# Kernel tuning notes

Hardware: AMD Instinct MI355X
Metric: run time of the kernel (lower is better)

## Reference

```python
import jax, jax.numpy as jnp
import numpy as np

B = 32          # batch_size
S = 64          # num_subgraph
D = 8           # dim_multi_hot (module-level global in source repo)
NE = S * D      # num_edges = 512
NNODES = 1024
E = 150000      # incidence rows
IN_UNITS = [16, 32, 32]
OUT_UNITS = [32, 32, 16]


def _glorot(key, shape):
    # glorot_normal over last two dims (out, in)
    fan_out, fan_in = shape[-2], shape[-1]
    std = (2.0 / (fan_in + fan_out)) ** 0.5
    return std * jax.random.normal(key, shape, dtype=jnp.float32)


def setup_inputs() -> dict:
    key = jax.random.key(0)
    ks = jax.random.split(key, 10)
    nodes_features = jax.random.normal(ks[0], (NNODES * S, IN_UNITS[0]), dtype=jnp.float32)
    c0 = jax.random.randint(ks[1], (E,), 0, B, dtype=jnp.int32)
    c1 = jax.random.randint(ks[2], (E,), 0, NNODES, dtype=jnp.int32)
    c2 = jax.random.randint(ks[3], (E,), 0, S, dtype=jnp.int32)
    c3 = jax.random.randint(ks[4], (E,), 0, D, dtype=jnp.int32)
    incidence_matrix = jnp.stack([c0, c1, c2, c3], axis=1)
    return {
        'nodes_features': nodes_features,
        'in_core0': _glorot(ks[5], (NE, IN_UNITS[1], IN_UNITS[0])),
        'in_bias0': jnp.zeros((NE, IN_UNITS[1], 1), jnp.float32),
        'in_core1': _glorot(ks[6], (NE, IN_UNITS[2], IN_UNITS[1])),
        'in_bias1': jnp.zeros((NE, IN_UNITS[2], 1), jnp.float32),
        'out_core0': _glorot(ks[7], (NE, OUT_UNITS[1], OUT_UNITS[0])),
        'out_bias0': jnp.zeros((NE, OUT_UNITS[1], 1), jnp.float32),
        'out_core1': _glorot(ks[8], (NE, OUT_UNITS[2], OUT_UNITS[1])),
        'out_bias1': jnp.zeros((NE, OUT_UNITS[2], 1), jnp.float32),
        'incidence_matrix': incidence_matrix,
    }


def reference(nodes_features, in_core0, in_bias0, in_core1, in_bias1,
              out_core0, out_bias0, out_core1, out_bias1, incidence_matrix):
    c0 = incidence_matrix[:, 0]
    c1 = incidence_matrix[:, 1]
    c2 = incidence_matrix[:, 2]
    c3 = incidence_matrix[:, 3]

    # gather node features per incidence row: [E, in0]
    x = nodes_features[c1 * S + c2]
    eidx = c2 * D + c3  # per-edge weight index, < NE

    # per-edge MLP (gathered batched matmul + bias + relu)
    for W, b in ((in_core0, in_bias0), (in_core1, in_bias1)):
        x = jax.nn.relu(jnp.einsum('eoi,ei->eo', W[eidx], x) + b[eidx, :, 0])

    # unsorted segment mean over irregular edge groups
    seg = c0 * (D * S) + c2 * D + c3
    nseg = B * S * D
    sums = jax.ops.segment_sum(x, seg, num_segments=nseg)           # [B*NE, 32]
    cnt = jax.ops.segment_sum(jnp.ones((x.shape[0], 1), x.dtype), seg, num_segments=nseg)
    ef = jnp.where(cnt > 0, sums / jnp.maximum(cnt, 1.0), 0.0)       # [B*NE, 32]

    # output MLP: weights tiled over batch (einsum avoids explicit repeat)
    ef = ef.reshape(B, NE, -1)
    for W, b in ((out_core0, out_bias0), (out_core1, out_bias1)):
        ef = jax.nn.relu(jnp.einsum('eoi,bei->beo', W, ef) + b[None, :, :, 0])

    return ef.reshape(B * NE, OUT_UNITS[-1], 1)
```

## Files before the change

### kernel.cpp

```cpp
#include <hip/hip_runtime.h>

#define B_    32
#define S_    64
#define D_    8
#define NE_   512
#define E_    150000
#define CAP   448

#define SBLK  1024
#define BLKN  ((E_ + SBLK - 1) / SBLK)
#define SLOTS 16
#define PBIN_PITCH (BLKN * SLOTS)

#define PAYLOAD_BYTE_OFF (NE_ * BLKN * 4)

typedef __attribute__((ext_vector_type(8)))  short  short8;
typedef __attribute__((ext_vector_type(16))) float  float16;

__device__ __forceinline__ unsigned short f2bf(float f) {
    union { float f; unsigned int u; } cv; cv.f = f;
    unsigned int u = cv.u;
    return (unsigned short)((u + 0x7fffu + ((u >> 16) & 1u)) >> 16);
}
__device__ __forceinline__ unsigned int pack2bf(float a, float b) {
    return (unsigned int)f2bf(a) | ((unsigned int)f2bf(b) << 16);
}

__global__ __launch_bounds__(SBLK)
void scatter_bin(const int* __restrict__ inc,
                 int* __restrict__ cnt2D,
                 int* __restrict__ payload2D) {
    __shared__ int lcount[NE_];
    const int tid = threadIdx.x;

    for (int i = tid; i < NE_; i += SBLK) lcount[i] = 0;
    __syncthreads();

    const int e = blockIdx.x * SBLK + tid;
    int ei = -1, lp = 0, pl = 0;
    if (e < E_) {
        const int4 c = ((const int4*)inc)[e];
        ei = c.z * D_ + c.w;
        pl = (c.x << 16) | (c.y * S_ + c.z);
        lp = atomicAdd(&lcount[ei], 1);
    }
    if (ei >= 0 && lp < SLOTS)
        payload2D[ei * PBIN_PITCH + blockIdx.x * SLOTS + lp] = pl;
    __syncthreads();
    if (tid < NE_)
        cnt2D[tid * BLKN + blockIdx.x] = min(lcount[tid], SLOTS);
}

#define HLP 40

__global__ __launch_bounds__(512, 4)
void main_mfma(const float* __restrict__ nf,
               const float* __restrict__ iw0, const float* __restrict__ ib0,
               const float* __restrict__ iw1, const float* __restrict__ ib1,
               const float* __restrict__ ow0, const float* __restrict__ ob0,
               const float* __restrict__ ow1, const float* __restrict__ ob1,
               const int* __restrict__ cnt2D, const int* __restrict__ payload2D,
               float* __restrict__ out) {
    const int bid  = blockIdx.x;
    const int tid  = threadIdx.x;
    const int lane = tid & 63;
    const int wav  = tid >> 6;
    const int e32  = lane & 31;
    const int q    = lane >> 5;

    __shared__ float acc[32][33];
    __shared__ float hb[32][33];
    __shared__ float cnts[32];
    __shared__ float q0t[32 * 33];
    __shared__ float q1t[32 * 17];
    __shared__ float qb0s[32], qb1s[16];
    __shared__ float bias0s[32], bias1s[32];
    __shared__ int   scnt[256];
    __shared__ int   elist[CAP];
    __shared__ unsigned short Hl[8][32 * HLP];

    short8 aWa, aWb0, aWb1;
    {
        const float* wa = iw0 + (size_t)bid * 512 + e32 * 16 + q * 8;
        float4 u0 = ((const float4*)wa)[0], u1 = ((const float4*)wa)[1];
        unsigned int p[4] = { pack2bf(u0.x,u0.y), pack2bf(u0.z,u0.w),
                              pack2bf(u1.x,u1.y), pack2bf(u1.z,u1.w) };
        aWa = *(short8*)p;
    }
    {
        const float* wb = iw1 + (size_t)bid * 1024 + e32 * 32 + q * 8;
        float4 u0 = ((const float4*)wb)[0], u1 = ((const float4*)wb)[1];
        unsigned int p[4] = { pack2bf(u0.x,u0.y), pack2bf(u0.z,u0.w),
                              pack2bf(u1.x,u1.y), pack2bf(u1.z,u1.w) };
        aWb0 = *(short8*)p;
        const float* wb2 = wb + 16;
        float4 u2 = ((const float4*)wb2)[0], u3 = ((const float4*)wb2)[1];
        unsigned int p2[4] = { pack2bf(u2.x,u2.y), pack2bf(u2.z,u2.w),
                               pack2bf(u3.x,u3.y), pack2bf(u3.z,u3.w) };
        aWb1 = *(short8*)p2;
    }

    int mycnt = 0;
    if (tid < BLKN) mycnt = cnt2D[bid * BLKN + tid];
    if (tid < 256)  scnt[tid] = (tid < BLKN) ? mycnt : 0;

    for (int i = tid; i < 1024; i += 512) {
        const int o = i >> 5, k = i & 31;
        q0t[k * 33 + o] = ow0[(size_t)bid * 1024 + i];
    }
    { const int o = tid >> 5, k = tid & 31;
      q1t[k * 17 + o] = ow1[(size_t)bid * 512 + tid]; }
    if (tid < 32)       { bias0s[tid] = ib0[bid * 32 + tid]; cnts[tid] = 0.f; }
    else if (tid < 64)  bias1s[tid - 32] = ib1[bid * 32 + (tid - 32)];
    else if (tid < 96)  qb0s[tid - 64] = ob0[bid * 32 + (tid - 64)];
    else if (tid < 112) qb1s[tid - 96] = ob1[bid * 16 + (tid - 96)];
    for (int i = tid; i < 32 * 33; i += 512) ((float*)acc)[i] = 0.f;
    __syncthreads();

    #pragma unroll
    for (int off = 1; off < 256; off <<= 1) {
        int v = 0;
        if (tid < 256) { v = scnt[tid]; if (tid >= off) v += scnt[tid - off]; }
        __syncthreads();
        if (tid < 256) scnt[tid] = v;
        __syncthreads();
    }
    const int n = min(scnt[BLKN - 1], CAP);

    const int* Pb = payload2D + (size_t)bid * PBIN_PITCH;
    for (int pair = tid; pair < PBIN_PITCH; pair += 512) {
        const int blk = pair >> 4, s = pair & (SLOTS - 1);
        const int b0 = blk ? scnt[blk - 1] : 0;
        const int cc = scnt[blk] - b0;
        if (s < cc) {
            const int idx = b0 + s;
            if (idx < CAP) elist[idx] = Pb[pair];
        }
    }
    __syncthreads();

    const int ntiles = (n + 31) >> 5;
    unsigned short* hl = Hl[wav];

    for (int t = wav; t < ntiles; t += 8) {
        const int slot  = t * 32 + e32;
        const bool valid = slot < n;
        const int cs    = valid ? slot : (n - 1);

        const int p   = elist[cs];
        const int b_e = p >> 16;
        const int row = p & 0xFFFF;

        short8 bX;
        {
            const float4* xp = (const float4*)(nf + (size_t)row * 16 + q * 8);
            float4 u0 = xp[0], u1 = xp[1];
            unsigned int pk[4] = { pack2bf(u0.x,u0.y), pack2bf(u0.z,u0.w),
                                   pack2bf(u1.x,u1.y), pack2bf(u1.z,u1.w) };
            bX = *(short8*)pk;
        }

        float16 c0;
        #pragma unroll
        for (int r = 0; r < 16; ++r) {
            const int o_r = (r & 3) + 8 * (r >> 2) + 4 * q;
            c0[r] = bias0s[o_r];
        }
        c0 = __builtin_amdgcn_mfma_f32_32x32x16_bf16(aWa, bX, c0, 0, 0, 0);

        #pragma unroll
        for (int r = 0; r < 16; r += 2) {
            const int o_r = (r & 3) + 8 * (r >> 2) + 4 * q;
            const unsigned int pk = pack2bf(fmaxf(c0[r], 0.f), fmaxf(c0[r + 1], 0.f));
            *(unsigned int*)(hl + e32 * HLP + o_r) = pk;
        }

        short8 bH0 = *(const short8*)(hl + e32 * HLP + q * 8);
        short8 bH1 = *(const short8*)(hl + e32 * HLP + 16 + q * 8);
        float16 c1;
        #pragma unroll
        for (int r = 0; r < 16; ++r) {
            const int o_r = (r & 3) + 8 * (r >> 2) + 4 * q;
            c1[r] = bias1s[o_r];
        }
        c1 = __builtin_amdgcn_mfma_f32_32x32x16_bf16(aWb0, bH0, c1, 0, 0, 0);
        c1 = __builtin_amdgcn_mfma_f32_32x32x16_bf16(aWb1, bH1, c1, 0, 0, 0);

        if (valid) {
            #pragma unroll
            for (int r = 0; r < 16; ++r) {
                const int o_r = (r & 3) + 8 * (r >> 2) + 4 * q;
                atomicAdd(&acc[b_e][o_r], fmaxf(c1[r], 0.f));
            }
            if (q == 0) atomicAdd(&cnts[b_e], 1.f);
        }
    }
    __syncthreads();

    {
        const int b  = tid >> 4;
        const int j  = tid & 15;
        const float cv  = cnts[b];
        const float inv = cv > 0.f ? 1.0f / cv : 0.0f;
        #pragma unroll
        for (int s = 0; s < 2; ++s) {
            const int oo = j * 2 + s;
            float d = 0.f;
            #pragma unroll
            for (int k = 0; k < 32; ++k) d = fmaf(q0t[k * 33 + oo], acc[b][k], d);
            hb[b][oo] = fmaxf(fmaf(d, inv, qb0s[oo]), 0.f);
        }
    }
    __syncthreads();

    {
        const int b = tid >> 4;
        const int o = tid & 15;
        float d = qb1s[o];
        #pragma unroll
        for (int k = 0; k < 32; ++k) d = fmaf(q1t[k * 17 + o], hb[b][k], d);
        out[((size_t)b * NE_ + bid) * 16 + o] = fmaxf(d, 0.f);
    }
}

extern "C" void kernel_launch(void* const* d_in, const int* in_sizes, int n_in,
                              void* d_out, int out_size, void* d_ws, size_t ws_size,
                              hipStream_t stream) {
    const float* nf  = (const float*)d_in[0];
    const float* iw0 = (const float*)d_in[1];
    const float* ib0 = (const float*)d_in[2];
    const float* iw1 = (const float*)d_in[3];
    const float* ib1 = (const float*)d_in[4];
    const float* ow0 = (const float*)d_in[5];
    const float* ob0 = (const float*)d_in[6];
    const float* ow1 = (const float*)d_in[7];
    const float* ob1 = (const float*)d_in[8];
    const int*   inc = (const int*)d_in[9];

    int* cnt2D     = (int*)d_ws;
    int* payload2D = (int*)((char*)d_ws + PAYLOAD_BYTE_OFF);

    scatter_bin<<<BLKN, SBLK, 0, stream>>>(inc, cnt2D, payload2D);
    main_mfma<<<NE_, 512, 0, stream>>>(nf, iw0, ib0, iw1, ib1, ow0, ob0, ow1, ob1,
                                       cnt2D, payload2D, (float*)d_out);
}
```

Baseline: 118.4 us.

## Replace per-block bins with global-atomic CSR scatter and register-only MLP tiles

The scatter kernel now reserves contiguous slots per edge with one global atomicAdd per block and edge bin, writing a compact CAP-sized list per edge. This removes the prefix scan and compaction in the main kernel. The main kernel prefetches at most two tiles per wave up front. It replaces the LDS round-trip between the two MLP layers with v_permlane32_swap register shuffles. The changes add a memset launch and global atomics, and they assume at most 16 tiles per edge (n ≤ 448), which CAP enforces.

```diff
diff --git a/kernel.cpp b/kernel.cpp
--- a/kernel.cpp
+++ b/kernel.cpp
@@ -7,12 +7,8 @@
 #define E_    150000
 #define CAP   448
 
-#define SBLK  1024
-#define BLKN  ((E_ + SBLK - 1) / SBLK)
-#define SLOTS 16
-#define PBIN_PITCH (BLKN * SLOTS)
-
-#define PAYLOAD_BYTE_OFF (NE_ * BLKN * 4)
+#define SC_BLK  1024
+#define SC_GRID ((E_ + SC_BLK - 1) / SC_BLK)
 
 typedef __attribute__((ext_vector_type(8)))  short  short8;
 typedef __attribute__((ext_vector_type(16))) float  float16;
@@ -26,17 +22,18 @@
     return (unsigned int)f2bf(a) | ((unsigned int)f2bf(b) << 16);
 }
 
-__global__ __launch_bounds__(SBLK)
-void scatter_bin(const int* __restrict__ inc,
-                 int* __restrict__ cnt2D,
-                 int* __restrict__ payload2D) {
+__global__ __launch_bounds__(SC_BLK)
+void scatter_csr(const int* __restrict__ inc,
+                 int* __restrict__ gcnt,
+                 int* __restrict__ payload) {
     __shared__ int lcount[NE_];
+    __shared__ int lbase[NE_];
     const int tid = threadIdx.x;
 
-    for (int i = tid; i < NE_; i += SBLK) lcount[i] = 0;
-    __syncthreads();
-
-    const int e = blockIdx.x * SBLK + tid;
+    if (tid < NE_) lcount[tid] = 0;
+    __syncthreads();
+
+    const int e = blockIdx.x * SC_BLK + tid;
     int ei = -1, lp = 0, pl = 0;
     if (e < E_) {
         const int4 c = ((const int4*)inc)[e];
@@ -44,14 +41,54 @@
         pl = (c.x << 16) | (c.y * S_ + c.z);
         lp = atomicAdd(&lcount[ei], 1);
     }
-    if (ei >= 0 && lp < SLOTS)
-        payload2D[ei * PBIN_PITCH + blockIdx.x * SLOTS + lp] = pl;
-    __syncthreads();
-    if (tid < NE_)
-        cnt2D[tid * BLKN + blockIdx.x] = min(lcount[tid], SLOTS);
-}
-
-#define HLP 40
+    __syncthreads();
+
+    if (tid < NE_) {
+        const int c = lcount[tid];
+        lbase[tid] = c ? atomicAdd(&gcnt[tid], c) : 0;
+    }
+    __syncthreads();
+
+    if (ei >= 0) {
+        const int s = lbase[ei] + lp;
+        if (s < CAP) payload[ei * CAP + s] = pl;
+    }
+}
+
+
+#define TILE_COMPUTE(bXv, pvv, vldv)                                            \
+  {                                                                             \
+    float16 c0;                                                                 \
+    _Pragma("unroll")                                                           \
+    for (int r = 0; r < 16; ++r)                                                \
+        c0[r] = bias0s[(r & 3) + 8 * (r >> 2) + 4 * q];                         \
+    c0 = __builtin_amdgcn_mfma_f32_32x32x16_bf16(aWa, (bXv), c0, 0, 0, 0);      \
+    unsigned Pw[8];                                                             \
+    _Pragma("unroll")                                                           \
+    for (int j = 0; j < 8; ++j)                                                 \
+        Pw[j] = pack2bf(fmaxf(c0[2 * j], 0.f), fmaxf(c0[2 * j + 1], 0.f));      \
+    asm("v_permlane32_swap_b32 %0, %1" : "+v"(Pw[0]), "+v"(Pw[2]));             \
+    asm("v_permlane32_swap_b32 %0, %1" : "+v"(Pw[1]), "+v"(Pw[3]));             \
+    asm("v_permlane32_swap_b32 %0, %1" : "+v"(Pw[4]), "+v"(Pw[6]));             \
+    asm("v_permlane32_swap_b32 %0, %1" : "+v"(Pw[5]), "+v"(Pw[7]));             \
+    union { unsigned u[4]; short8 s; } H0c, H1c;                                \
+    H0c.u[0] = Pw[0]; H0c.u[1] = Pw[1]; H0c.u[2] = Pw[2]; H0c.u[3] = Pw[3];     \
+    H1c.u[0] = Pw[4]; H1c.u[1] = Pw[5]; H1c.u[2] = Pw[6]; H1c.u[3] = Pw[7];     \
+    float16 c1;                                                                 \
+    _Pragma("unroll")                                                           \
+    for (int r = 0; r < 16; ++r)                                                \
+        c1[r] = bias1s[(r & 3) + 8 * (r >> 2) + 4 * q];                         \
+    c1 = __builtin_amdgcn_mfma_f32_32x32x16_bf16(aWb0, H0c.s, c1, 0, 0, 0);     \
+    c1 = __builtin_amdgcn_mfma_f32_32x32x16_bf16(aWb1, H1c.s, c1, 0, 0, 0);     \
+    if (vldv) {                                                                 \
+        const int b_e = ((pvv) >> 16) & 31;                                     \
+        _Pragma("unroll")                                                       \
+        for (int r = 0; r < 16; ++r)                                            \
+            atomicAdd(&acc[b_e][(r & 3) + 8 * (r >> 2) + 4 * q],                \
+                      fmaxf(c1[r], 0.f));                                       \
+        if (q == 0) atomicAdd(&cnts[b_e], 1.f);                                 \
+    }                                                                           \
+  }
 
 __global__ __launch_bounds__(512, 4)
 void main_mfma(const float* __restrict__ nf,
@@ -59,7 +96,7 @@
                const float* __restrict__ iw1, const float* __restrict__ ib1,
                const float* __restrict__ ow0, const float* __restrict__ ob0,
                const float* __restrict__ ow1, const float* __restrict__ ob1,
-               const int* __restrict__ cnt2D, const int* __restrict__ payload2D,
+               const int* __restrict__ gcnt, const int* __restrict__ payload,
                float* __restrict__ out) {
     const int bid  = blockIdx.x;
     const int tid  = threadIdx.x;
@@ -75,9 +112,6 @@
     __shared__ float q1t[32 * 17];
     __shared__ float qb0s[32], qb1s[16];
     __shared__ float bias0s[32], bias1s[32];
-    __shared__ int   scnt[256];
-    __shared__ int   elist[CAP];
-    __shared__ unsigned short Hl[8][32 * HLP];
 
     short8 aWa, aWb0, aWb1;
     {
@@ -100,10 +134,6 @@
         aWb1 = *(short8*)p2;
     }
 
-    int mycnt = 0;
-    if (tid < BLKN) mycnt = cnt2D[bid * BLKN + tid];
-    if (tid < 256)  scnt[tid] = (tid < BLKN) ? mycnt : 0;
-
     for (int i = tid; i < 1024; i += 512) {
         const int o = i >> 5, k = i & 31;
         q0t[k * 33 + o] = ow0[(size_t)bid * 1024 + i];
@@ -115,86 +145,42 @@
     else if (tid < 96)  qb0s[tid - 64] = ob0[bid * 32 + (tid - 64)];
     else if (tid < 112) qb1s[tid - 96] = ob1[bid * 16 + (tid - 96)];
     for (int i = tid; i < 32 * 33; i += 512) ((float*)acc)[i] = 0.f;
-    __syncthreads();
-
-    #pragma unroll
-    for (int off = 1; off < 256; off <<= 1) {
-        int v = 0;
-        if (tid < 256) { v = scnt[tid]; if (tid >= off) v += scnt[tid - off]; }
-        __syncthreads();
-        if (tid < 256) scnt[tid] = v;
-        __syncthreads();
-    }
-    const int n = min(scnt[BLKN - 1], CAP);
-
-    const int* Pb = payload2D + (size_t)bid * PBIN_PITCH;
-    for (int pair = tid; pair < PBIN_PITCH; pair += 512) {
-        const int blk = pair >> 4, s = pair & (SLOTS - 1);
-        const int b0 = blk ? scnt[blk - 1] : 0;
-        const int cc = scnt[blk] - b0;
-        if (s < cc) {
-            const int idx = b0 + s;
-            if (idx < CAP) elist[idx] = Pb[pair];
-        }
-    }
-    __syncthreads();
-
+
+    const int n = min(gcnt[bid], CAP);
     const int ntiles = (n + 31) >> 5;
-    unsigned short* hl = Hl[wav];
-
-    for (int t = wav; t < ntiles; t += 8) {
-        const int slot  = t * 32 + e32;
-        const bool valid = slot < n;
-        const int cs    = valid ? slot : (n - 1);
-
-        const int p   = elist[cs];
-        const int b_e = p >> 16;
-        const int row = p & 0xFFFF;
-
-        short8 bX;
-        {
-            const float4* xp = (const float4*)(nf + (size_t)row * 16 + q * 8);
-            float4 u0 = xp[0], u1 = xp[1];
-            unsigned int pk[4] = { pack2bf(u0.x,u0.y), pack2bf(u0.z,u0.w),
-                                   pack2bf(u1.x,u1.y), pack2bf(u1.z,u1.w) };
-            bX = *(short8*)pk;
-        }
-
-        float16 c0;
-        #pragma unroll
-        for (int r = 0; r < 16; ++r) {
-            const int o_r = (r & 3) + 8 * (r >> 2) + 4 * q;
-            c0[r] = bias0s[o_r];
-        }
-        c0 = __builtin_amdgcn_mfma_f32_32x32x16_bf16(aWa, bX, c0, 0, 0, 0);
-
-        #pragma unroll
-        for (int r = 0; r < 16; r += 2) {
-            const int o_r = (r & 3) + 8 * (r >> 2) + 4 * q;
-            const unsigned int pk = pack2bf(fmaxf(c0[r], 0.f), fmaxf(c0[r + 1], 0.f));
-            *(unsigned int*)(hl + e32 * HLP + o_r) = pk;
-        }
-
-        short8 bH0 = *(const short8*)(hl + e32 * HLP + q * 8);
-        short8 bH1 = *(const short8*)(hl + e32 * HLP + 16 + q * 8);
-        float16 c1;
-        #pragma unroll
-        for (int r = 0; r < 16; ++r) {
-            const int o_r = (r & 3) + 8 * (r >> 2) + 4 * q;
-            c1[r] = bias1s[o_r];
-        }
-        c1 = __builtin_amdgcn_mfma_f32_32x32x16_bf16(aWb0, bH0, c1, 0, 0, 0);
-        c1 = __builtin_amdgcn_mfma_f32_32x32x16_bf16(aWb1, bH1, c1, 0, 0, 0);
-
-        if (valid) {
-            #pragma unroll
-            for (int r = 0; r < 16; ++r) {
-                const int o_r = (r & 3) + 8 * (r >> 2) + 4 * q;
-                atomicAdd(&acc[b_e][o_r], fmaxf(c1[r], 0.f));
-            }
-            if (q == 0) atomicAdd(&cnts[b_e], 1.f);
-        }
-    }
+    const bool h0 = wav < ntiles;
+    const bool h1 = (wav + 8) < ntiles;
+    int  pv0 = 0, pv1 = 0;
+    bool v0 = false, v1 = false;
+    short8 bX0 = {}, bX1 = {};
+    if (h0) {
+        const int s = (wav << 5) + e32;
+        v0 = s < n;
+        pv0 = payload[bid * CAP + (v0 ? s : n - 1)];
+    }
+    if (h1) {
+        const int s = ((wav + 8) << 5) + e32;
+        v1 = s < n;
+        pv1 = payload[bid * CAP + (v1 ? s : n - 1)];
+    }
+    if (h0) {
+        const float4* xp = (const float4*)(nf + (size_t)(pv0 & 0xFFFF) * 16 + q * 8);
+        float4 u0 = xp[0], u1 = xp[1];
+        unsigned int pk[4] = { pack2bf(u0.x,u0.y), pack2bf(u0.z,u0.w),
+                               pack2bf(u1.x,u1.y), pack2bf(u1.z,u1.w) };
+        bX0 = *(short8*)pk;
+    }
+    if (h1) {
+        const float4* xp = (const float4*)(nf + (size_t)(pv1 & 0xFFFF) * 16 + q * 8);
+        float4 u0 = xp[0], u1 = xp[1];
+        unsigned int pk[4] = { pack2bf(u0.x,u0.y), pack2bf(u0.z,u0.w),
+                               pack2bf(u1.x,u1.y), pack2bf(u1.z,u1.w) };
+        bX1 = *(short8*)pk;
+    }
+    __syncthreads();
+
+    if (h0) TILE_COMPUTE(bX0, pv0, v0);
+    if (h1) TILE_COMPUTE(bX1, pv1, v1);
     __syncthreads();
 
     {
@@ -237,10 +223,11 @@
     const float* ob1 = (const float*)d_in[8];
     const int*   inc = (const int*)d_in[9];
 
-    int* cnt2D     = (int*)d_ws;
-    int* payload2D = (int*)((char*)d_ws + PAYLOAD_BYTE_OFF);
-
-    scatter_bin<<<BLKN, SBLK, 0, stream>>>(inc, cnt2D, payload2D);
+    int* gcnt    = (int*)d_ws;
+    int* payload = (int*)((char*)d_ws + 4096);
+
+    hipMemsetAsync(gcnt, 0, NE_ * sizeof(int), stream);
+    scatter_csr<<<SC_GRID, SC_BLK, 0, stream>>>(inc, gcnt, payload);
     main_mfma<<<NE_, 512, 0, stream>>>(nf, iw0, ib0, iw1, ib1, ow0, ob0, ow1, ob1,
-                                       cnt2D, payload2D, (float*)d_out);
-}
+                                       gcnt, payload, (float*)d_out);
+}
```

New measurement: 120.8 us. 1.02x slower.
